# Optimization experiments

Hardware: AMD Instinct MI355X
Metric: run time of the kernel (lower is better)

## Reference

```python
import jax, jax.numpy as jnp
import numpy as np

N, H, M, D = 128, 512, 2048, 128  # batch, dim_h_o, dim_C2_1, dim_C2_2
EPS = 1e-8
LN2 = float(np.log(2.0))


def _cos_sim(a, b, eps=EPS):
    # torch.nn.CosineSimilarity over last dim with eps clamp on norms
    num = jnp.sum(a * b, axis=-1)
    na = jnp.maximum(jnp.sqrt(jnp.sum(a * a, axis=-1)), eps)
    nb = jnp.maximum(jnp.sqrt(jnp.sum(b * b, axis=-1)), eps)
    return num / (na * nb)


def setup_inputs() -> dict:
    key = jax.random.key(0)
    ks = jax.random.split(key, 16)
    s = 0.02
    return {
        "h_o_prev": jax.random.normal(ks[0], (N, H), jnp.float32),
        "c_prev": jax.random.normal(ks[1], (N, M, D), jnp.float32),
        "c_xf": jax.random.normal(ks[2], (N, M, D), jnp.float32),
        "Wk": jax.random.normal(ks[3], (D, H), jnp.float32) * s,
        "bk": jnp.zeros((D,), jnp.float32),
        "Wb": jax.random.normal(ks[4], (1, H), jnp.float32) * s,
        "bb": jnp.zeros((1,), jnp.float32),
        "We": jax.random.normal(ks[5], (D, H), jnp.float32) * s,
        "be": jnp.zeros((D,), jnp.float32),
        "Wv": jax.random.normal(ks[6], (D, H), jnp.float32) * s,
        "bv": jnp.zeros((D,), jnp.float32),
        "W_ih": jax.random.normal(ks[7], (3 * H, D), jnp.float32) * s,
        "W_hh": jax.random.normal(ks[8], (3 * H, H), jnp.float32) * s,
        "b_ih": jnp.zeros((3 * H,), jnp.float32),
        "b_hh": jnp.zeros((3 * H,), jnp.float32),
    }


def _gru_cell(x, h, W_ih, W_hh, b_ih, b_hh):
    # torch GRUCell: gates ordered (reset, update, new)
    gi = x @ W_ih.T + b_ih
    gh = h @ W_hh.T + b_hh
    i_r, i_z, i_n = jnp.split(gi, 3, axis=-1)
    h_r, h_z, h_n = jnp.split(gh, 3, axis=-1)
    r = jax.nn.sigmoid(i_r + h_r)
    z = jax.nn.sigmoid(i_z + h_z)
    n = jnp.tanh(i_n + r * h_n)
    return (1.0 - z) * n + z * h


def reference(h_o_prev, c_prev, c_xf, Wk, bk, Wb, bb, We, be, Wv, bv, W_ih, W_hh, b_ih, b_hh):
    # key / key-strength
    k = h_o_prev @ Wk.T + bk                       # [N, D]
    beta_pre = h_o_prev @ Wb.T + bb                # [N, 1]
    beta_pos = jnp.maximum(beta_pre, 0.0)
    beta_neg = jnp.minimum(beta_pre, 0.0)
    beta = (jnp.log1p(jnp.exp(beta_neg)) + beta_pos
            + jnp.log1p(jnp.exp(-beta_pos)) + (1.0 - LN2))  # softplus(x)+1

    # read addressing over c_xf
    s_kx = _cos_sim(c_xf, k[:, None, :])           # [N, M]
    w_kx = jax.nn.softmax(s_kx * beta, axis=1)     # [N, M]
    r = jnp.einsum('nm,nmd->nd', w_kx, c_xf)       # [N, D]

    # write addressing over c_prev
    s_kc = _cos_sim(c_prev, k[:, None, :])         # [N, M]
    w_kc = jax.nn.softmax(s_kc * beta, axis=1)     # [N, M]

    # controller update
    h_o = _gru_cell(r, h_o_prev, W_ih, W_hh, b_ih, b_hh)  # [N, H]

    # erase / add memory write
    e = jax.nn.sigmoid(h_o @ We.T + be)            # [N, D]
    v = h_o @ Wv.T + bv                            # [N, D]
    w2 = w_kc[:, :, None]                          # [N, M, 1]
    c_new = c_prev * (1.0 - w2 * e[:, None, :]) + w2 * v[:, None, :]
    return (h_o, c_new)
```

## Files before the change

### kernel.cpp

```cpp
#include <hip/hip_runtime.h>
#include <math.h>

#define NN 128
#define HH 512
#define MM 2048
#define DD 128
#define EPSF 1e-8f


__global__ void k1_kbeta(const float* __restrict__ h, const float* __restrict__ Wk,
                         const float* __restrict__ bk, const float* __restrict__ Wb,
                         const float* __restrict__ bb, float* __restrict__ k,
                         float* __restrict__ kn, float* __restrict__ beta) {
    int n = blockIdx.x;
    int t = threadIdx.x;
    __shared__ float hs[HH];
    __shared__ float red[128];
    for (int i = t; i < HH; i += 128) hs[i] = h[n * HH + i];
    __syncthreads();
    float acc = bk[t];
    const float* wr = Wk + t * HH;
    for (int hh = 0; hh < HH; hh += 4) {
        float4 w4 = *(const float4*)(wr + hh);
        acc += w4.x * hs[hh] + w4.y * hs[hh + 1] + w4.z * hs[hh + 2] + w4.w * hs[hh + 3];
    }
    k[n * DD + t] = acc;
    red[t] = acc * acc;
    __syncthreads();
    for (int s = 64; s > 0; s >>= 1) { if (t < s) red[t] += red[t + s]; __syncthreads(); }
    if (t == 0) kn[n] = fmaxf(sqrtf(red[0]), EPSF);
    __syncthreads();
    float b = 0.f;
    for (int i = t; i < HH; i += 128) b += hs[i] * Wb[i];
    red[t] = b;
    __syncthreads();
    for (int s = 64; s > 0; s >>= 1) { if (t < s) red[t] += red[t + s]; __syncthreads(); }
    if (t == 0) {
        float bp   = red[0] + bb[0];
        float bpos = fmaxf(bp, 0.f);
        float bneg = fminf(bp, 0.f);
        beta[n] = log1pf(expf(bneg)) + bpos + log1pf(expf(-bpos))
                + (1.f - 0.69314718055994530942f);
    }
}

__global__ void kA_scores(const float* __restrict__ c_prev, const float* __restrict__ c_xf,
                          const float* __restrict__ kv, const float* __restrict__ kn,
                          const float* __restrict__ beta,
                          float* __restrict__ sc, float* __restrict__ rp,
                          float* __restrict__ cmx, float* __restrict__ clx,
                          float* __restrict__ cmc, float* __restrict__ clc) {
    int b     = blockIdx.x;
    int arr   = b & 1;
    int chunk = (b >> 1) & 31;
    int n     = b >> 6;
    int t     = threadIdx.x;
    __shared__ float tile[64 * 128];
    __shared__ float kl[128];
    __shared__ float redD[256];
    __shared__ float redN[256];
    __shared__ float ps[64];

    const float*  src  = arr ? c_prev : c_xf;
    const float4* src4 = (const float4*)src + (size_t)(n * MM + chunk * 64) * 32;
    #pragma unroll
    for (int i = 0; i < 8; i++) {
        int fid = t + 256 * i;
        int row = fid >> 5, c4 = fid & 31;
        float4 vld = src4[fid];
        int c4s = c4 ^ (row & 7);
        *(float4*)&tile[row * 128 + c4s * 4] = vld;
    }
    if (t < 128) kl[t] = kv[n * DD + t];
    __syncthreads();
    float sb = beta[n] / kn[n];

    int row = t & 63, q = t >> 6;
    float dk = 0.f, nn = 0.f;
    #pragma unroll
    for (int j = 0; j < 8; j++) {
        int g  = q * 8 + j;
        int gs = g ^ (row & 7);
        float4 cv = *(const float4*)&tile[row * 128 + gs * 4];
        float4 kk = *(const float4*)&kl[g * 4];
        dk += cv.x * kk.x + cv.y * kk.y + cv.z * kk.z + cv.w * kk.w;
        nn += cv.x * cv.x + cv.y * cv.y + cv.z * cv.z + cv.w * cv.w;
    }
    redD[t] = dk; redN[t] = nn;
    __syncthreads();
    float s = 0.f;
    if (t < 64) {
        dk = redD[t] + redD[t + 64] + redD[t + 128] + redD[t + 192];
        nn = redN[t] + redN[t + 64] + redN[t + 128] + redN[t + 192];
        s  = dk / fmaxf(sqrtf(nn), EPSF) * sb;
        if (arr) sc[n * MM + chunk * 64 + t] = s;
    }
    __syncthreads();
    redD[t] = (t < 64) ? s : -1e30f;
    __syncthreads();
    for (int st = 32; st >= 1; st >>= 1) {
        if (t < st) redD[t] = fmaxf(redD[t], redD[t + st]);
        __syncthreads();
    }
    float mu = redD[0];
    if (t < 64) { float p = expf(s - mu); ps[t] = p; redN[t] = p; }
    __syncthreads();
    for (int st = 32; st >= 1; st >>= 1) {
        if (t < st) redN[t] += redN[t + st];
        __syncthreads();
    }
    float lb = redN[0];

    if (arr) {
        if (t == 0) { cmc[n * 32 + chunk] = mu; clc[n * 32 + chunk] = lb; }
        return;
    }
    int d = t & 127, half = t >> 7;
    float acc = 0.f;
    #pragma unroll 8
    for (int m = 0; m < 32; m++) {
        int mm  = half * 32 + m;
        int idx = mm * 128 + (((d >> 2) ^ (mm & 7)) << 2) + (d & 3);
        acc += ps[mm] * tile[idx];
    }
    redD[t] = acc;
    __syncthreads();
    if (t < 128) rp[((size_t)n * 32 + chunk) * 128 + t] = redD[t] + redD[t + 128];
    if (t == 0) { cmx[n * 32 + chunk] = mu; clx[n * 32 + chunk] = lb; }
}

__global__ void kB_combine(const float* __restrict__ rp, const float* __restrict__ cmx,
                           const float* __restrict__ clx, const float* __restrict__ cmc,
                           const float* __restrict__ clc, float* __restrict__ r,
                           float* __restrict__ muc, float* __restrict__ invLc) {
    int n = blockIdx.x;
    int t = threadIdx.x;
    float mu = -1e30f;
    for (int c = 0; c < 32; c++) mu = fmaxf(mu, cmx[n * 32 + c]);
    float L = 0.f, acc = 0.f;
    for (int c = 0; c < 32; c++) {
        float w = expf(cmx[n * 32 + c] - mu);
        L   += w * clx[n * 32 + c];
        acc += w * rp[((size_t)n * 32 + c) * 128 + t];
    }
    r[n * DD + t] = acc / L;
    if (t == 0) {
        float m2 = -1e30f;
        for (int c = 0; c < 32; c++) m2 = fmaxf(m2, cmc[n * 32 + c]);
        float L2 = 0.f;
        for (int c = 0; c < 32; c++) L2 += expf(cmc[n * 32 + c] - m2) * clc[n * 32 + c];
        muc[n] = m2; invLc[n] = 1.f / L2;
    }
}

__global__ void g1_gemm(const float* __restrict__ rf, const float* __restrict__ h,
                        const float* __restrict__ Wih, const float* __restrict__ Whh,
                        const float* __restrict__ bih, const float* __restrict__ bhh,
                        float* __restrict__ A, float* __restrict__ B) {
    int bI = blockIdx.x;
    int jt = bI % 96, nt = bI / 96;
    int t  = threadIdx.x;
    int tn = t & 15, tj = t >> 4;
    int n  = nt * 16 + tn;
    int j  = jt * 16 + tj;
    __shared__ float act[16][132];
    __shared__ float wt[16][132];
    int lbase = t * 8;
    int lrow  = lbase >> 7, lcol = lbase & 127;
    float accA = 0.f, accB = 0.f;
    for (int c = 0; c < 5; ++c) {
        if (c == 0) {
            int gn = nt * 16 + lrow;
            const float4* s = (const float4*)(rf + gn * DD + lcol);
            *(float4*)&act[lrow][lcol]     = s[0];
            *(float4*)&act[lrow][lcol + 4] = s[1];
            const float4* w = (const float4*)(Wih + (jt * 16 + lrow) * DD + lcol);
            *(float4*)&wt[lrow][lcol]      = w[0];
            *(float4*)&wt[lrow][lcol + 4]  = w[1];
        } else {
            int koff = (c - 1) * 128;
            const float4* s = (const float4*)(h + (nt * 16 + lrow) * HH + koff + lcol);
            *(float4*)&act[lrow][lcol]     = s[0];
            *(float4*)&act[lrow][lcol + 4] = s[1];
            const float4* w = (const float4*)(Whh + (jt * 16 + lrow) * HH + koff + lcol);
            *(float4*)&wt[lrow][lcol]      = w[0];
            *(float4*)&wt[lrow][lcol + 4]  = w[1];
        }
        __syncthreads();
        float acc = 0.f;
        const float* ar = act[tn];
        const float* wr = wt[tj];
        #pragma unroll
        for (int kk = 0; kk < 128; kk += 4) {
            float4 a4 = *(const float4*)(ar + kk);
            float4 w4 = *(const float4*)(wr + kk);
            acc += a4.x * w4.x + a4.y * w4.y + a4.z * w4.z + a4.w * w4.w;
        }
        if (c == 0) accA = acc; else accB += acc;
        __syncthreads();
    }
    A[n * 1536 + j] = accA + bih[j];
    B[n * 1536 + j] = accB + bhh[j];
}

__global__ void g2_gates(const float* __restrict__ A, const float* __restrict__ B,
                         const float* __restrict__ hprev, float* __restrict__ ho) {
    int id = blockIdx.x * 256 + threadIdx.x;
    int n = id >> 9, j = id & 511;
    const float* a = A + n * 1536;
    const float* b = B + n * 1536;
    float ir = a[j], iz = a[512 + j], in_ = a[1024 + j];
    float hr = b[j], hz = b[512 + j], hn  = b[1024 + j];
    float rg = 1.f / (1.f + expf(-(ir + hr)));
    float zg = 1.f / (1.f + expf(-(iz + hz)));
    float ng = tanhf(in_ + rg * hn);
    ho[id] = (1.f - zg) * ng + zg * hprev[id];
}

__global__ void g3_ev(const float* __restrict__ ho, const float* __restrict__ We,
                      const float* __restrict__ be, const float* __restrict__ Wv,
                      const float* __restrict__ bv, float* __restrict__ e,
                      float* __restrict__ v) {
    int bI = blockIdx.x;
    int jt = bI % 16, nt = bI / 16;
    int t  = threadIdx.x;
    int tn = t & 15, tj = t >> 4;
    int n  = nt * 16 + tn;
    int j  = jt * 16 + tj;
    __shared__ float act[16][132];
    __shared__ float wt[16][132];
    int lbase = t * 8;
    int lrow  = lbase >> 7, lcol = lbase & 127;
    int wrow  = jt * 16 + lrow;
    const float* Wsrc = (wrow < 128) ? (We + wrow * HH) : (Wv + (wrow - 128) * HH);
    float acc = 0.f;
    for (int c = 0; c < 4; ++c) {
        int koff = c * 128;
        const float4* s = (const float4*)(ho + (nt * 16 + lrow) * HH + koff + lcol);
        *(float4*)&act[lrow][lcol]     = s[0];
        *(float4*)&act[lrow][lcol + 4] = s[1];
        const float4* w = (const float4*)(Wsrc + koff + lcol);
        *(float4*)&wt[lrow][lcol]      = w[0];
        *(float4*)&wt[lrow][lcol + 4]  = w[1];
        __syncthreads();
        const float* ar = act[tn];
        const float* wr = wt[tj];
        #pragma unroll
        for (int kk = 0; kk < 128; kk += 4) {
            float4 a4 = *(const float4*)(ar + kk);
            float4 w4 = *(const float4*)(wr + kk);
            acc += a4.x * w4.x + a4.y * w4.y + a4.z * w4.z + a4.w * w4.w;
        }
        __syncthreads();
    }
    if (j < 128) e[n * DD + j] = 1.f / (1.f + expf(-(acc + be[j])));
    else         v[n * DD + (j - 128)] = acc + bv[j - 128];
}

__global__ void k6_cnew(const float* __restrict__ c_prev, const float* __restrict__ sc,
                        const float* __restrict__ muc, const float* __restrict__ invLc,
                        const float* __restrict__ e, const float* __restrict__ v,
                        float* __restrict__ out) {
    int i  = blockIdx.x * 256 + threadIdx.x;
    int nm = i >> 5;
    int d4 = i & 31;
    int n  = nm >> 11;
    float w = expf(sc[nm] - muc[n]) * invLc[n];
    float4 c4 = ((const float4*)c_prev)[i];
    float4 e4 = ((const float4*)e)[n * 32 + d4];
    float4 v4 = ((const float4*)v)[n * 32 + d4];
    float4 o;
    o.x = c4.x * (1.f - w * e4.x) + w * v4.x;
    o.y = c4.y * (1.f - w * e4.y) + w * v4.y;
    o.z = c4.z * (1.f - w * e4.z) + w * v4.z;
    o.w = c4.w * (1.f - w * e4.w) + w * v4.w;
    ((float4*)out)[i] = o;
}

extern "C" void kernel_launch(void* const* d_in, const int* in_sizes, int n_in,
                              void* d_out, int out_size, void* d_ws, size_t ws_size,
                              hipStream_t stream) {
    const float* h_o_prev = (const float*)d_in[0];
    const float* c_prev   = (const float*)d_in[1];
    const float* c_xf     = (const float*)d_in[2];
    const float* Wk       = (const float*)d_in[3];
    const float* bk       = (const float*)d_in[4];
    const float* Wb       = (const float*)d_in[5];
    const float* bb       = (const float*)d_in[6];
    const float* We       = (const float*)d_in[7];
    const float* be       = (const float*)d_in[8];
    const float* Wv       = (const float*)d_in[9];
    const float* bv       = (const float*)d_in[10];
    const float* Wih      = (const float*)d_in[11];
    const float* Whh      = (const float*)d_in[12];
    const float* bih      = (const float*)d_in[13];
    const float* bhh      = (const float*)d_in[14];

    float* ws    = (float*)d_ws;
    float* k     = ws;
    float* kn    = ws + 16384;
    float* beta  = ws + 16512;
    float* sc    = ws + 16640;
    float* rp    = ws + 278784;
    float* cmx   = ws + 803072;
    float* clx   = ws + 807168;
    float* cmc   = ws + 811264;
    float* clc   = ws + 815360;
    float* r     = ws + 819456;
    float* muc   = ws + 835840;
    float* invLc = ws + 835968;
    float* e     = ws + 836096;
    float* v     = ws + 852480;
    float* Ag    = ws + 278784;
    float* Bg    = ws + 475392;

    float* ho_out = (float*)d_out;
    float* c_out  = (float*)d_out + NN * HH;

    k1_kbeta<<<NN, 128, 0, stream>>>(h_o_prev, Wk, bk, Wb, bb, k, kn, beta);
    kA_scores<<<NN * 32 * 2, 256, 0, stream>>>(c_prev, c_xf, k, kn, beta,
                                               sc, rp, cmx, clx, cmc, clc);
    kB_combine<<<NN, 128, 0, stream>>>(rp, cmx, clx, cmc, clc, r, muc, invLc);
    g1_gemm<<<768, 256, 0, stream>>>(r, h_o_prev, Wih, Whh, bih, bhh, Ag, Bg);
    g2_gates<<<NN * HH / 256, 256, 0, stream>>>(Ag, Bg, h_o_prev, ho_out);
    g3_ev<<<128, 256, 0, stream>>>(ho_out, We, be, Wv, bv, e, v);
    k6_cnew<<<NN * MM * DD / 4 / 256, 256, 0, stream>>>(c_prev, sc, muc, invLc, e, v, c_out);
}
```

Baseline: 143.7 us.

## Split score kernel into per-array kernels with register tiles and shuffle reductions

Replaces the combined score kernel, which staged a 32KB swizzled LDS tile and used tree reductions with many barriers, with two specialised kernels. One handles c_prev and the other c_xf. Each keeps its rows in registers and reduces dot products and norms with wave shuffles, and only the c_xf kernel computes the weighted read vector. This cuts LDS traffic, barrier count and shared memory per block to raise occupancy. The cost is higher register pressure in the c_xf kernel, which holds eight float4 rows, plus one extra kernel launch.

```diff
diff --git a/kernel.cpp b/kernel.cpp
--- a/kernel.cpp
+++ b/kernel.cpp
@@ -44,89 +44,119 @@
     }
 }
 
-__global__ void kA_scores(const float* __restrict__ c_prev, const float* __restrict__ c_xf,
-                          const float* __restrict__ kv, const float* __restrict__ kn,
-                          const float* __restrict__ beta,
-                          float* __restrict__ sc, float* __restrict__ rp,
-                          float* __restrict__ cmx, float* __restrict__ clx,
-                          float* __restrict__ cmc, float* __restrict__ clc) {
-    int b     = blockIdx.x;
-    int arr   = b & 1;
-    int chunk = (b >> 1) & 31;
-    int n     = b >> 6;
-    int t     = threadIdx.x;
-    __shared__ float tile[64 * 128];
-    __shared__ float kl[128];
-    __shared__ float redD[256];
-    __shared__ float redN[256];
+__global__ void kP_prev(const float* __restrict__ c_prev, const float* __restrict__ kv,
+                        const float* __restrict__ kn, const float* __restrict__ beta,
+                        float* __restrict__ sc, float* __restrict__ cmc,
+                        float* __restrict__ clc) {
+    int b = blockIdx.x;
+    int chunk = b & 31, n = b >> 5;
+    int t = threadIdx.x;
+    int w = t >> 5, c = t & 31;
     __shared__ float ps[64];
-
-    const float*  src  = arr ? c_prev : c_xf;
-    const float4* src4 = (const float4*)src + (size_t)(n * MM + chunk * 64) * 32;
-    #pragma unroll
-    for (int i = 0; i < 8; i++) {
-        int fid = t + 256 * i;
-        int row = fid >> 5, c4 = fid & 31;
-        float4 vld = src4[fid];
-        int c4s = c4 ^ (row & 7);
-        *(float4*)&tile[row * 128 + c4s * 4] = vld;
-    }
-    if (t < 128) kl[t] = kv[n * DD + t];
-    __syncthreads();
+    float4 k4 = *(const float4*)(kv + n * DD + 4 * c);
+    const float4* src4 = (const float4*)c_prev + (size_t)(n * MM + chunk * 64) * 32;
+    float dk[8], nn[8];
+    #pragma unroll
+    for (int i = 0; i < 8; i++) {
+        float4 x = src4[t + 256 * i];
+        dk[i] = x.x * k4.x + x.y * k4.y + x.z * k4.z + x.w * k4.w;
+        nn[i] = x.x * x.x + x.y * x.y + x.z * x.z + x.w * x.w;
+    }
+    #pragma unroll
+    for (int m = 1; m < 32; m <<= 1) {
+        #pragma unroll
+        for (int i = 0; i < 8; i++) {
+            dk[i] += __shfl_xor(dk[i], m, 32);
+            nn[i] += __shfl_xor(nn[i], m, 32);
+        }
+    }
     float sb = beta[n] / kn[n];
-
-    int row = t & 63, q = t >> 6;
-    float dk = 0.f, nn = 0.f;
-    #pragma unroll
-    for (int j = 0; j < 8; j++) {
-        int g  = q * 8 + j;
-        int gs = g ^ (row & 7);
-        float4 cv = *(const float4*)&tile[row * 128 + gs * 4];
-        float4 kk = *(const float4*)&kl[g * 4];
-        dk += cv.x * kk.x + cv.y * kk.y + cv.z * kk.z + cv.w * kk.w;
-        nn += cv.x * cv.x + cv.y * cv.y + cv.z * cv.z + cv.w * cv.w;
-    }
-    redD[t] = dk; redN[t] = nn;
-    __syncthreads();
-    float s = 0.f;
+    #pragma unroll
+    for (int i = 0; i < 8; i++) {
+        if (c == i) {
+            float s = dk[i] / fmaxf(sqrtf(nn[i]), EPSF) * sb;
+            ps[w + 8 * i] = s;
+            sc[n * MM + chunk * 64 + w + 8 * i] = s;
+        }
+    }
+    __syncthreads();
     if (t < 64) {
-        dk = redD[t] + redD[t + 64] + redD[t + 128] + redD[t + 192];
-        nn = redN[t] + redN[t + 64] + redN[t + 128] + redN[t + 192];
-        s  = dk / fmaxf(sqrtf(nn), EPSF) * sb;
-        if (arr) sc[n * MM + chunk * 64 + t] = s;
-    }
-    __syncthreads();
-    redD[t] = (t < 64) ? s : -1e30f;
-    __syncthreads();
-    for (int st = 32; st >= 1; st >>= 1) {
-        if (t < st) redD[t] = fmaxf(redD[t], redD[t + st]);
-        __syncthreads();
-    }
-    float mu = redD[0];
-    if (t < 64) { float p = expf(s - mu); ps[t] = p; redN[t] = p; }
-    __syncthreads();
-    for (int st = 32; st >= 1; st >>= 1) {
-        if (t < st) redN[t] += redN[t + st];
-        __syncthreads();
-    }
-    float lb = redN[0];
-
-    if (arr) {
-        if (t == 0) { cmc[n * 32 + chunk] = mu; clc[n * 32 + chunk] = lb; }
-        return;
-    }
-    int d = t & 127, half = t >> 7;
-    float acc = 0.f;
-    #pragma unroll 8
-    for (int m = 0; m < 32; m++) {
-        int mm  = half * 32 + m;
-        int idx = mm * 128 + (((d >> 2) ^ (mm & 7)) << 2) + (d & 3);
-        acc += ps[mm] * tile[idx];
-    }
-    redD[t] = acc;
-    __syncthreads();
-    if (t < 128) rp[((size_t)n * 32 + chunk) * 128 + t] = redD[t] + redD[t + 128];
-    if (t == 0) { cmx[n * 32 + chunk] = mu; clx[n * 32 + chunk] = lb; }
+        float s = ps[t];
+        float mu = s;
+        #pragma unroll
+        for (int m = 1; m < 64; m <<= 1) mu = fmaxf(mu, __shfl_xor(mu, m, 64));
+        float p = expf(s - mu);
+        #pragma unroll
+        for (int m = 1; m < 64; m <<= 1) p += __shfl_xor(p, m, 64);
+        if (t == 0) { cmc[n * 32 + chunk] = mu; clc[n * 32 + chunk] = p; }
+    }
+}
+
+__global__ void kX_xf(const float* __restrict__ c_xf, const float* __restrict__ kv,
+                      const float* __restrict__ kn, const float* __restrict__ beta,
+                      float* __restrict__ rp, float* __restrict__ cmx,
+                      float* __restrict__ clx) {
+    int b = blockIdx.x;
+    int chunk = b & 31, n = b >> 5;
+    int t = threadIdx.x;
+    int w = t >> 5, c = t & 31;
+    __shared__ float ps[64];
+    __shared__ float part[4 * 128];
+    float4 k4 = *(const float4*)(kv + n * DD + 4 * c);
+    const float4* src4 = (const float4*)c_xf + (size_t)(n * MM + chunk * 64) * 32;
+    float4 x[8];
+    float dk[8], nn[8];
+    #pragma unroll
+    for (int i = 0; i < 8; i++) {
+        x[i] = src4[t + 256 * i];
+        dk[i] = x[i].x * k4.x + x[i].y * k4.y + x[i].z * k4.z + x[i].w * k4.w;
+        nn[i] = x[i].x * x[i].x + x[i].y * x[i].y + x[i].z * x[i].z + x[i].w * x[i].w;
+    }
+    #pragma unroll
+    for (int m = 1; m < 32; m <<= 1) {
+        #pragma unroll
+        for (int i = 0; i < 8; i++) {
+            dk[i] += __shfl_xor(dk[i], m, 32);
+            nn[i] += __shfl_xor(nn[i], m, 32);
+        }
+    }
+    float sb = beta[n] / kn[n];
+    #pragma unroll
+    for (int i = 0; i < 8; i++) {
+        if (c == i) ps[w + 8 * i] = dk[i] / fmaxf(sqrtf(nn[i]), EPSF) * sb;
+    }
+    __syncthreads();
+    if (t < 64) {
+        float s = ps[t];
+        float mu = s;
+        #pragma unroll
+        for (int m = 1; m < 64; m <<= 1) mu = fmaxf(mu, __shfl_xor(mu, m, 64));
+        float p = expf(s - mu);
+        ps[t] = p;
+        float lb = p;
+        #pragma unroll
+        for (int m = 1; m < 64; m <<= 1) lb += __shfl_xor(lb, m, 64);
+        if (t == 0) { cmx[n * 32 + chunk] = mu; clx[n * 32 + chunk] = lb; }
+    }
+    __syncthreads();
+    float4 acc = {0.f, 0.f, 0.f, 0.f};
+    #pragma unroll
+    for (int i = 0; i < 8; i++) {
+        float p = ps[w + 8 * i];
+        acc.x += p * x[i].x; acc.y += p * x[i].y;
+        acc.z += p * x[i].z; acc.w += p * x[i].w;
+    }
+    acc.x += __shfl_xor(acc.x, 32, 64);
+    acc.y += __shfl_xor(acc.y, 32, 64);
+    acc.z += __shfl_xor(acc.z, 32, 64);
+    acc.w += __shfl_xor(acc.w, 32, 64);
+    int ww = t >> 6;
+    if ((t & 63) < 32) *(float4*)&part[ww * 128 + 4 * c] = acc;
+    __syncthreads();
+    if (t < 128) {
+        float a = part[t] + part[128 + t] + part[256 + t] + part[384 + t];
+        rp[((size_t)n * 32 + chunk) * 128 + t] = a;
+    }
 }
 
 __global__ void kB_combine(const float* __restrict__ rp, const float* __restrict__ cmx,
@@ -318,8 +348,8 @@
     float* c_out  = (float*)d_out + NN * HH;
 
     k1_kbeta<<<NN, 128, 0, stream>>>(h_o_prev, Wk, bk, Wb, bb, k, kn, beta);
-    kA_scores<<<NN * 32 * 2, 256, 0, stream>>>(c_prev, c_xf, k, kn, beta,
-                                               sc, rp, cmx, clx, cmc, clc);
+    kP_prev<<<NN * 32, 256, 0, stream>>>(c_prev, k, kn, beta, sc, cmc, clc);
+    kX_xf<<<NN * 32, 256, 0, stream>>>(c_xf, k, kn, beta, rp, cmx, clx);
     kB_combine<<<NN, 128, 0, stream>>>(rp, cmx, clx, cmc, clc, r, muc, invLc);
     g1_gemm<<<768, 256, 0, stream>>>(r, h_o_prev, Wih, Whh, bih, bhh, Ag, Bg);
     g2_gates<<<NN * HH / 256, 256, 0, stream>>>(Ag, Bg, h_o_prev, ho_out);
```

After: 157.1 us. +9.4%, slower.
